# Performance work log

Measured on AMD Instinct MI355X. Metric: run time of the kernel, lower is better.

## Reference

```python
import jax, jax.numpy as jnp
import numpy as np

NUM_GROUPS1 = 8
NUM_GROUPS2 = 4
NUM_HEADS = 8


def setup_inputs() -> dict:
    key = jax.random.key(0)
    k1, k2, k3 = jax.random.split(key, 3)
    B, N, C = 8, 4096, 512
    x = jax.random.normal(k1, (B, N, C), dtype=jnp.float32)
    # torch Linear(dim, 3*inner_dim, bias=False); stored transposed for x @ W
    W_qkv = jax.random.normal(k2, (C, 3 * C), dtype=jnp.float32) * 0.02
    W_proj = jax.random.normal(k3, (C, C), dtype=jnp.float32) * 0.02
    b_proj = jnp.zeros((C,), dtype=jnp.float32)
    return {"x": x, "W_qkv": W_qkv, "W_proj": W_proj, "b_proj": b_proj,
            "recursive_index": 0}


def reference(x, W_qkv, W_proj, b_proj, recursive_index):
    # recursive_index is a static Python int (0 -> False branch, num_groups1).
    num_groups = NUM_GROUPS1 if not recursive_index else NUM_GROUPS2
    B, N, C = x.shape
    H = NUM_HEADS
    Dh = C // H
    scale = Dh ** -0.5
    Np = int(np.ceil(N / num_groups) * num_groups)
    if Np != N:
        x = jnp.pad(x, ((0, 0), (0, Np - N), (0, 0)))
    L = Np // num_groups  # tokens per group
    # qkv projection, then split into per-group per-head tensors [B,G,H,L,Dh]
    qkv = (x @ W_qkv).reshape(B, num_groups, L, 3, H, Dh)
    q = jnp.transpose(qkv[:, :, :, 0], (0, 1, 3, 2, 4))
    k = jnp.transpose(qkv[:, :, :, 1], (0, 1, 3, 2, 4))
    v = jnp.transpose(qkv[:, :, :, 2], (0, 1, 3, 2, 4))
    attn = jax.nn.softmax(jnp.einsum('bghld,bghmd->bghlm', q, k) * scale, axis=-1)
    out = jnp.einsum('bghlm,bghmd->bghld', attn, v)  # [B,G,H,L,Dh]
    out = jnp.transpose(out, (0, 1, 3, 2, 4)).reshape(B, Np, C)[:, :N]
    return out @ W_proj + b_proj
```

## Files before the change

kernel.cpp:

```cpp
#include <hip/hip_runtime.h>
#include <hip/hip_bf16.h>

typedef __attribute__((ext_vector_type(8))) short  bf16x8;
typedef __attribute__((ext_vector_type(4))) float  f32x4;

__device__ __forceinline__ ushort f2bf(float f) {
    unsigned u = __builtin_bit_cast(unsigned, f);
    u += 0x7fffu + ((u >> 16) & 1u);
    return (ushort)(u >> 16);
}

__device__ __forceinline__ void gload_lds16(const ushort* g, ushort* l) {
    __builtin_amdgcn_global_load_lds(
        (const __attribute__((address_space(1))) void*)(g),
        (__attribute__((address_space(3))) void*)(l), 16, 0, 0);
}

__global__ __launch_bounds__(256) void prep_kernel(
        const float* __restrict__ x, ushort* __restrict__ xb,
        const float* __restrict__ Wqkv, ushort* __restrict__ wq,
        const float* __restrict__ Wproj, ushort* __restrict__ wp) {
    __shared__ ushort t[64 * 65];
    const int bx = blockIdx.x, tid = threadIdx.x;
    if (bx < 16384) {
        int i = bx * 256 + tid;
        float4 f = reinterpret_cast<const float4*>(x)[i];
        ushort4 o;
        o.x = f2bf(f.x); o.y = f2bf(f.y); o.z = f2bf(f.z); o.w = f2bf(f.w);
        reinterpret_cast<ushort4*>(xb)[i] = o;
        return;
    }
    const float* in; ushort* out; int Cc, qcols, cB, rB; float qs;
    if (bx < 16576) {
        int b2 = bx - 16384;
        in = Wqkv; out = wq; Cc = 1536; qcols = 512;
        qs = 0.18033688011112043f;
        cB = (b2 % 24) * 64; rB = (b2 / 24) * 64;
    } else {
        int b2 = bx - 16576;
        in = Wproj; out = wp; Cc = 512; qcols = 0; qs = 1.0f;
        cB = (b2 % 8) * 64; rB = (b2 / 8) * 64;
    }
#pragma unroll
    for (int p = 0; p < 16; ++p) {
        int lin = p * 256 + tid;
        int r = lin >> 6, c = lin & 63;
        float v = in[(size_t)(rB + r) * Cc + cB + c];
        if (cB + c < qcols) v *= qs;
        t[c * 65 + r] = f2bf(v);
    }
    __syncthreads();
#pragma unroll
    for (int p = 0; p < 16; ++p) {
        int lin = p * 256 + tid;
        int c = lin >> 6, r = lin & 63;
        out[(size_t)(cB + c) * 512 + rB + r] = t[c * 65 + r];
    }
}

template<bool F32OUT, bool SPLIT_VT>
__global__ __launch_bounds__(256) void gemm_bt_kernel(
        const ushort* __restrict__ A, const ushort* __restrict__ Bt,
        void* __restrict__ Cout, const float* __restrict__ bias,
        const ushort* __restrict__ Wv, ushort* __restrict__ vT,
        int Ncols, int K) {
    __shared__ ushort smem[16384];
    ushort* la = smem;
    ushort* lb = smem + 8192;
    const int tid  = threadIdx.x;
    const int id = blockIdx.x;
    const bool vt = SPLIT_VT && (id >= 2048);
    const ushort* Amat; const ushort* Bmat; int mBase, nBase;
    if (!vt) {
        Amat = A; Bmat = Bt;
        mBase = ((id & 7) * 32 + ((id >> 3) & 31)) << 7;
        nBase = (id >> 8) << 7;
    } else {
        int vid = id - 2048;
        Amat = Wv; Bmat = A;
        mBase = (vid >> 8) << 7;
        nBase = ((vid & 7) * 32 + ((vid >> 3) & 31)) << 7;
    }
    const int w = tid >> 6, lane = tid & 63, ml = lane & 15, quad = lane >> 4;
    const int wr = (w >> 1) << 6, wc = (w & 1) << 6;

    const int srow = lane >> 3;
    const int sch  = (lane & 7) ^ srow;
    const ushort* Ap = Amat + (size_t)(mBase + w * 32 + srow) * K + sch * 8;
    const ushort* Bp = Bmat + (size_t)(nBase + w * 32 + srow) * K + sch * 8;
    ushort* lA0 = la + (w * 32) * 64;
    ushort* lB0 = lb + (w * 32) * 64;

    f32x4 z4 = {0.f, 0.f, 0.f, 0.f};
    f32x4 acc[4][4];
#pragma unroll
    for (int i = 0; i < 4; ++i)
#pragma unroll
        for (int j = 0; j < 4; ++j) acc[i][j] = z4;

    const int nkt = K >> 6;
    for (int kt = 0; kt < nkt; ++kt) {
#pragma unroll
        for (int i = 0; i < 4; ++i) {
            gload_lds16(Ap + (size_t)(8 * i) * K, lA0 + (8 * i) * 64);
            gload_lds16(Bp + (size_t)(8 * i) * K, lB0 + (8 * i) * 64);
        }
        Ap += 64; Bp += 64;
        __syncthreads();
#pragma unroll
        for (int ks = 0; ks < 2; ++ks) {
            bf16x8 af[4], bv[4];
#pragma unroll
            for (int i = 0; i < 4; ++i)
                af[i] = *reinterpret_cast<bf16x8*>(
                    la + (wr + i * 16 + ml) * 64 + (((ks * 4 + quad) ^ (ml & 7)) << 3));
#pragma unroll
            for (int j = 0; j < 4; ++j)
                bv[j] = *reinterpret_cast<bf16x8*>(
                    lb + (wc + j * 16 + ml) * 64 + (((ks * 4 + quad) ^ (ml & 7)) << 3));
#pragma unroll
            for (int i = 0; i < 4; ++i)
#pragma unroll
                for (int j = 0; j < 4; ++j)
                    acc[i][j] = __builtin_amdgcn_mfma_f32_16x16x32_bf16(af[i], bv[j], acc[i][j], 0, 0, 0);
        }
        __syncthreads();
    }

    if (F32OUT) {
        float* ep = reinterpret_cast<float*>(smem) + w * 1088;
        float bj[4];
#pragma unroll
        for (int j = 0; j < 4; ++j) bj[j] = bias[nBase + wc + j * 16 + ml];
        float* cbase = reinterpret_cast<float*>(Cout);
#pragma unroll
        for (int i = 0; i < 4; ++i) {
#pragma unroll
            for (int j = 0; j < 4; ++j)
#pragma unroll
                for (int r = 0; r < 4; ++r)
                    ep[(quad * 4 + r) * 68 + j * 16 + ml] = acc[i][j][r] + bj[j];
#pragma unroll
            for (int t = 0; t < 4; ++t) {
                int ch = quad + 4 * t;
                float4 v = *reinterpret_cast<const float4*>(ep + ml * 68 + ch * 4);
                *reinterpret_cast<float4*>(cbase
                    + (size_t)(mBase + wr + i * 16 + ml) * Ncols + nBase + wc + ch * 4) = v;
            }
        }
    } else {
        ushort* ep = smem + w * 1152;
#pragma unroll
        for (int i = 0; i < 4; ++i) {
#pragma unroll
            for (int j = 0; j < 4; ++j)
#pragma unroll
                for (int r = 0; r < 4; ++r)
                    ep[(quad * 4 + r) * 72 + j * 16 + ml] = f2bf(acc[i][j][r]);
#pragma unroll
            for (int t = 0; t < 2; ++t) {
                int ch = quad + 4 * t;
                bf16x8 v = *reinterpret_cast<const bf16x8*>(ep + ml * 72 + ch * 8);
                int row = mBase + wr + i * 16 + ml;
                if (!vt) {
                    *reinterpret_cast<bf16x8*>(reinterpret_cast<ushort*>(Cout)
                        + (size_t)row * Ncols + nBase + wc + ch * 8) = v;
                } else {
                    *reinterpret_cast<bf16x8*>(vT
                        + ((size_t)((nBase >> 9) * 512 + row)) * 512
                        + (nBase & 511) + wc + ch * 8) = v;
                }
            }
        }
    }
}

__global__ __launch_bounds__(256) void attn_kernel(
        const ushort* __restrict__ qk, const ushort* __restrict__ vT,
        ushort* __restrict__ out) {
    __shared__ ushort k_lds[64 * 64];
    __shared__ ushort v_lds[64 * 64];
    __shared__ ushort p_lds[4 * 32 * 72];
    const int tid = threadIdx.x;
    const int w = tid >> 6, lane = tid & 63, ml = lane & 15, quad = lane >> 4;
    const int id = blockIdx.x;
    const int bgh = id >> 2, qc = id & 3;
    const int b = bgh >> 6, g = (bgh >> 3) & 7, h = bgh & 7;
    const int tb = b * 4096 + g * 512;
    const ushort* base  = qk + (size_t)tb * 1024 + h * 64;
    const ushort* vbase = vT + ((size_t)((b * 8 + g) * 512 + h * 64)) * 512;
    const int qOff = qc * 128 + w * 32;

    bf16x8 qf[2][2];
#pragma unroll
    for (int qb = 0; qb < 2; ++qb)
#pragma unroll
        for (int ks = 0; ks < 2; ++ks)
            qf[qb][ks] = *reinterpret_cast<const bf16x8*>(
                base + (size_t)(qOff + qb * 16 + ml) * 1024 + ks * 32 + quad * 8);

    const int srow = lane >> 3;
    const int sch  = (lane & 7) ^ srow;
    const ushort* kp = base + (size_t)(w * 16 + srow) * 1024 + 512 + sch * 8;
    ushort* kdst = k_lds + (w * 16) * 64;
    const ushort* vp = vbase + (size_t)(w * 16 + srow) * 512 + sch * 8;
    ushort* vdst = v_lds + (w * 16) * 64;

    f32x4 z4 = {0.f, 0.f, 0.f, 0.f};
    f32x4 oacc[2][4];
    float lp[2];
#pragma unroll
    for (int qb = 0; qb < 2; ++qb) {
#pragma unroll
        for (int db = 0; db < 4; ++db) oacc[qb][db] = z4;
        lp[qb] = 0.f;
    }

    ushort* pw = p_lds + w * 32 * 72;
    for (int kt = 0; kt < 8; ++kt) {
        gload_lds16(kp + (size_t)(kt * 64) * 1024,     kdst);
        gload_lds16(kp + (size_t)(kt * 64 + 8) * 1024, kdst + 8 * 64);
        gload_lds16(vp + kt * 64,           vdst);
        gload_lds16(vp + 8 * 512 + kt * 64, vdst + 8 * 64);
        __syncthreads();

        f32x4 s[2][4];
#pragma unroll
        for (int qb = 0; qb < 2; ++qb)
#pragma unroll
            for (int kb = 0; kb < 4; ++kb) s[qb][kb] = z4;
#pragma unroll
        for (int ks = 0; ks < 2; ++ks) {
            bf16x8 kfs[4];
#pragma unroll
            for (int kb = 0; kb < 4; ++kb)
                kfs[kb] = *reinterpret_cast<bf16x8*>(
                    k_lds + (kb * 16 + ml) * 64 + (((ks * 4 + quad) ^ (ml & 7)) << 3));
#pragma unroll
            for (int qb = 0; qb < 2; ++qb)
#pragma unroll
                for (int kb = 0; kb < 4; ++kb)
                    s[qb][kb] = __builtin_amdgcn_mfma_f32_16x16x32_bf16(kfs[kb], qf[qb][ks], s[qb][kb], 0, 0, 0);
        }

#pragma unroll
        for (int qb = 0; qb < 2; ++qb)
#pragma unroll
            for (int kb = 0; kb < 4; ++kb) {
                float p0 = exp2f(s[qb][kb][0]), p1 = exp2f(s[qb][kb][1]);
                float p2 = exp2f(s[qb][kb][2]), p3 = exp2f(s[qb][kb][3]);
                lp[qb] += (p0 + p1) + (p2 + p3);
                ushort4 pk;
                pk.x = f2bf(p0); pk.y = f2bf(p1); pk.z = f2bf(p2); pk.w = f2bf(p3);
                *reinterpret_cast<ushort4*>(
                    pw + (qb * 16 + ml) * 72 + kb * 16 + quad * 4) = pk;
            }

#pragma unroll
        for (int ks = 0; ks < 2; ++ks) {
            bf16x8 pfs[2], vfs[4];
#pragma unroll
            for (int qb = 0; qb < 2; ++qb)
                pfs[qb] = *reinterpret_cast<bf16x8*>(
                    pw + (qb * 16 + ml) * 72 + ks * 32 + quad * 8);
#pragma unroll
            for (int db = 0; db < 4; ++db)
                vfs[db] = *reinterpret_cast<bf16x8*>(
                    v_lds + (db * 16 + ml) * 64 + (((ks * 4 + quad) ^ (ml & 7)) << 3));
#pragma unroll
            for (int qb = 0; qb < 2; ++qb)
#pragma unroll
                for (int db = 0; db < 4; ++db)
                    oacc[qb][db] = __builtin_amdgcn_mfma_f32_16x16x32_bf16(pfs[qb], vfs[db], oacc[qb][db], 0, 0, 0);
        }
        __syncthreads();
    }

    float invq[2][4];
#pragma unroll
    for (int qb = 0; qb < 2; ++qb) {
        float sline = lp[qb];
        sline += __shfl_xor(sline, 16);
        sline += __shfl_xor(sline, 32);
        float rinv = 1.0f / sline;
#pragma unroll
        for (int r = 0; r < 4; ++r)
            invq[qb][r] = __shfl(rinv, quad * 4 + r);
    }
#pragma unroll
    for (int qb = 0; qb < 2; ++qb)
#pragma unroll
        for (int db = 0; db < 4; ++db)
#pragma unroll
            for (int r = 0; r < 4; ++r) {
                float v = oacc[qb][db][r] * invq[qb][r];
                out[(size_t)(tb + qOff + qb * 16 + quad * 4 + r) * 512
                    + h * 64 + db * 16 + ml] = f2bf(v);
            }
}

extern "C" void kernel_launch(void* const* d_in, const int* in_sizes, int n_in,
                              void* d_out, int out_size, void* d_ws, size_t ws_size,
                              hipStream_t stream) {
    const float* x     = (const float*)d_in[0];
    const float* Wqkv  = (const float*)d_in[1];
    const float* Wproj = (const float*)d_in[2];
    const float* bproj = (const float*)d_in[3];

    char* ws = (char*)d_ws;
    ushort* xb   = (ushort*)(ws);
    ushort* wq   = (ushort*)(ws + 33554432);
    ushort* wp   = (ushort*)(ws + 35127296);
    ushort* qkb  = (ushort*)(ws + 35651584);
    ushort* vTb  = (ushort*)(ws + 102760448);
    ushort* attn = xb;
    ushort* wv   = wq + 1024 * 512;
    float*  outp = (float*)d_out;

    prep_kernel<<<16640, 256, 0, stream>>>(x, xb, Wqkv, wq, Wproj, wp);
    gemm_bt_kernel<false, true><<<3072, 256, 0, stream>>>(
        xb, wq, qkb, nullptr, wv, vTb, 1024, 512);
    attn_kernel<<<2048, 256, 0, stream>>>(qkb, vTb, attn);
    gemm_bt_kernel<true, false><<<1024, 256, 0, stream>>>(
        attn, wp, outp, bproj, nullptr, nullptr, 512, 512);
}
```

Measured before the change: 291.8 us.

## Double-buffer GEMM LDS tiles and compute softmax row sums with MFMA

The GEMM main loop now uses K-tiles of 32 with two LDS buffers and a new swizzle, prefetching the next tile while the current one is consumed, so there is one barrier per step instead of two. In the attention kernel, the row sums of P are computed by an extra MFMA against a ones vector, which removes the scalar accumulation and cross-lane shuffles. A hardware packed bf16 conversion instruction replaces the manual rounding. In exchange the GEMM runs twice as many shorter iterations, the attention kernel issues extra MFMAs, and the row sums now come from bf16-rounded P, which matches the numerator.

```diff
diff --git a/kernel.cpp b/kernel.cpp
--- a/kernel.cpp
+++ b/kernel.cpp
@@ -8,6 +8,12 @@
     unsigned u = __builtin_bit_cast(unsigned, f);
     u += 0x7fffu + ((u >> 16) & 1u);
     return (ushort)(u >> 16);
+}
+
+__device__ __forceinline__ unsigned cvt_pk_bf16(float a, float b) {
+    unsigned r;
+    asm("v_cvt_pk_bf16_f32 %0, %1, %2" : "=v"(r) : "v"(a), "v"(b));
+    return r;
 }
 
 __device__ __forceinline__ void gload_lds16(const ushort* g, ushort* l) {
@@ -65,8 +71,6 @@
         const ushort* __restrict__ Wv, ushort* __restrict__ vT,
         int Ncols, int K) {
     __shared__ ushort smem[16384];
-    ushort* la = smem;
-    ushort* lb = smem + 8192;
     const int tid  = threadIdx.x;
     const int id = blockIdx.x;
     const bool vt = SPLIT_VT && (id >= 2048);
@@ -84,12 +88,10 @@
     const int w = tid >> 6, lane = tid & 63, ml = lane & 15, quad = lane >> 4;
     const int wr = (w >> 1) << 6, wc = (w & 1) << 6;
 
-    const int srow = lane >> 3;
-    const int sch  = (lane & 7) ^ srow;
+    const int srow = lane >> 2;
+    const int sch  = (lane & 3) ^ ((lane >> 3) & 3);
     const ushort* Ap = Amat + (size_t)(mBase + w * 32 + srow) * K + sch * 8;
     const ushort* Bp = Bmat + (size_t)(nBase + w * 32 + srow) * K + sch * 8;
-    ushort* lA0 = la + (w * 32) * 64;
-    ushort* lB0 = lb + (w * 32) * 64;
 
     f32x4 z4 = {0.f, 0.f, 0.f, 0.f};
     f32x4 acc[4][4];
@@ -98,33 +100,40 @@
 #pragma unroll
         for (int j = 0; j < 4; ++j) acc[i][j] = z4;
 
-    const int nkt = K >> 6;
+    auto stagef = [&](int kt, int buf) {
+        ushort* la_ = smem + buf * 8192;
+        ushort* lb_ = la_ + 4096;
+        const ushort* a = Ap + kt * 32;
+        const ushort* b = Bp + kt * 32;
+        gload_lds16(a,            la_ + (w * 32) * 32);
+        gload_lds16(a + 16 * K,   la_ + (w * 32 + 16) * 32);
+        gload_lds16(b,            lb_ + (w * 32) * 32);
+        gload_lds16(b + 16 * K,   lb_ + (w * 32 + 16) * 32);
+    };
+
+    const int nkt = K >> 5;
+    const int rdoff = (quad ^ ((ml >> 1) & 3)) << 3;
+    stagef(0, 0);
+    __syncthreads();
+    int cur = 0;
     for (int kt = 0; kt < nkt; ++kt) {
-#pragma unroll
-        for (int i = 0; i < 4; ++i) {
-            gload_lds16(Ap + (size_t)(8 * i) * K, lA0 + (8 * i) * 64);
-            gload_lds16(Bp + (size_t)(8 * i) * K, lB0 + (8 * i) * 64);
-        }
-        Ap += 64; Bp += 64;
+        if (kt + 1 < nkt) stagef(kt + 1, cur ^ 1);
+        ushort* la_ = smem + cur * 8192;
+        ushort* lb_ = la_ + 4096;
+        bf16x8 af[4], bv[4];
+#pragma unroll
+        for (int i = 0; i < 4; ++i)
+            af[i] = *reinterpret_cast<bf16x8*>(la_ + (wr + i * 16 + ml) * 32 + rdoff);
+#pragma unroll
+        for (int j = 0; j < 4; ++j)
+            bv[j] = *reinterpret_cast<bf16x8*>(lb_ + (wc + j * 16 + ml) * 32 + rdoff);
+#pragma unroll
+        for (int i = 0; i < 4; ++i)
+#pragma unroll
+            for (int j = 0; j < 4; ++j)
+                acc[i][j] = __builtin_amdgcn_mfma_f32_16x16x32_bf16(af[i], bv[j], acc[i][j], 0, 0, 0);
         __syncthreads();
-#pragma unroll
-        for (int ks = 0; ks < 2; ++ks) {
-            bf16x8 af[4], bv[4];
-#pragma unroll
-            for (int i = 0; i < 4; ++i)
-                af[i] = *reinterpret_cast<bf16x8*>(
-                    la + (wr + i * 16 + ml) * 64 + (((ks * 4 + quad) ^ (ml & 7)) << 3));
-#pragma unroll
-            for (int j = 0; j < 4; ++j)
-                bv[j] = *reinterpret_cast<bf16x8*>(
-                    lb + (wc + j * 16 + ml) * 64 + (((ks * 4 + quad) ^ (ml & 7)) << 3));
-#pragma unroll
-            for (int i = 0; i < 4; ++i)
-#pragma unroll
-                for (int j = 0; j < 4; ++j)
-                    acc[i][j] = __builtin_amdgcn_mfma_f32_16x16x32_bf16(af[i], bv[j], acc[i][j], 0, 0, 0);
-        }
-        __syncthreads();
+        cur ^= 1;
     }
 
     if (F32OUT) {
@@ -206,14 +215,17 @@
     const ushort* vp = vbase + (size_t)(w * 16 + srow) * 512 + sch * 8;
     ushort* vdst = v_lds + (w * 16) * 64;
 
+    const bf16x8 onesf = {0x3f80, 0x3f80, 0x3f80, 0x3f80,
+                          0x3f80, 0x3f80, 0x3f80, 0x3f80};
+
     f32x4 z4 = {0.f, 0.f, 0.f, 0.f};
     f32x4 oacc[2][4];
-    float lp[2];
+    f32x4 sacc[2];
 #pragma unroll
     for (int qb = 0; qb < 2; ++qb) {
 #pragma unroll
         for (int db = 0; db < 4; ++db) oacc[qb][db] = z4;
-        lp[qb] = 0.f;
+        sacc[qb] = z4;
     }
 
     ushort* pw = p_lds + w * 32 * 72;
@@ -249,11 +261,11 @@
             for (int kb = 0; kb < 4; ++kb) {
                 float p0 = exp2f(s[qb][kb][0]), p1 = exp2f(s[qb][kb][1]);
                 float p2 = exp2f(s[qb][kb][2]), p3 = exp2f(s[qb][kb][3]);
-                lp[qb] += (p0 + p1) + (p2 + p3);
-                ushort4 pk;
-                pk.x = f2bf(p0); pk.y = f2bf(p1); pk.z = f2bf(p2); pk.w = f2bf(p3);
-                *reinterpret_cast<ushort4*>(
-                    pw + (qb * 16 + ml) * 72 + kb * 16 + quad * 4) = pk;
+                uint2 pk2;
+                pk2.x = cvt_pk_bf16(p0, p1);
+                pk2.y = cvt_pk_bf16(p2, p3);
+                *reinterpret_cast<uint2*>(
+                    pw + (qb * 16 + ml) * 72 + kb * 16 + quad * 4) = pk2;
             }
 
 #pragma unroll
@@ -267,6 +279,9 @@
             for (int db = 0; db < 4; ++db)
                 vfs[db] = *reinterpret_cast<bf16x8*>(
                     v_lds + (db * 16 + ml) * 64 + (((ks * 4 + quad) ^ (ml & 7)) << 3));
+#pragma unroll
+            for (int qb = 0; qb < 2; ++qb)
+                sacc[qb] = __builtin_amdgcn_mfma_f32_16x16x32_bf16(pfs[qb], onesf, sacc[qb], 0, 0, 0);
 #pragma unroll
             for (int qb = 0; qb < 2; ++qb)
 #pragma unroll
@@ -278,15 +293,10 @@
 
     float invq[2][4];
 #pragma unroll
-    for (int qb = 0; qb < 2; ++qb) {
-        float sline = lp[qb];
-        sline += __shfl_xor(sline, 16);
-        sline += __shfl_xor(sline, 32);
-        float rinv = 1.0f / sline;
+    for (int qb = 0; qb < 2; ++qb)
 #pragma unroll
         for (int r = 0; r < 4; ++r)
-            invq[qb][r] = __shfl(rinv, quad * 4 + r);
-    }
+            invq[qb][r] = 1.0f / sacc[qb][r];
 #pragma unroll
     for (int qb = 0; qb < 2; ++qb)
 #pragma unroll
```

Measured after the change: 299.6 us. +2.7%, slower.
